# Kernel optimization log

Measured on AMD Instinct MI355X. Metric: run time of the kernel, lower is better.

Reference implementation:

```python
import jax, jax.numpy as jnp
import numpy as np
import math

B, S, D, H = 4, 512, 1024, 16
DH = D // H
DQ = D // 4
MIN_STEPS, MAX_STEPS = 4, 12
THR = 1e-4


def lin(t, w, b):
    # torch Linear convention: w is (out, in)
    return jnp.einsum('...i,oi->...o', t, w) + b


def gelu(t):
    return jax.nn.gelu(t, approximate=False)  # torch nn.GELU() exact


def layernorm(t, g, b):
    m = t.mean(-1, keepdims=True)
    v = jnp.mean(jnp.square(t - m), axis=-1, keepdims=True)
    return (t - m) * jax.lax.rsqrt(v + 1e-5) * g + b


def _forward(h, x, ig_w1, ig_b1, ig_w2, ig_b2, wq, bq, wk, bk, wv, bv, wo, bo,
             g1_w1, g1_b1, g1_w2, g1_b2, gate_logits, ln_g, ln_b,
             sp_w1, sp_b1, sp_w2, sp_b2):
    # adaptive step count: steps = base + floor(sigmoid(MLP(mean_pool(h))).mean() * extra)
    pooled = h.mean(axis=1)  # (B, D)
    extra = jax.nn.sigmoid(lin(gelu(lin(pooled, sp_w1, sp_b1)), sp_w2, sp_b2)).mean()
    num_steps = jnp.minimum(
        MIN_STEPS + jnp.floor(extra * (MAX_STEPS - MIN_STEPS)).astype(jnp.int32), MAX_STEPS)

    gw = jax.nn.softmax(gate_logits)  # gate weights over the 3 gates
    scale = 1.0 / math.sqrt(DH)

    def step(carry, i):
        h, active = carry
        # G1 gate (G2/G3 multiply zero memory/expert outputs -> drop)
        G1 = jax.nn.sigmoid(lin(gelu(lin(h, g1_w1, g1_b1)), g1_w2, g1_b2)) * gw[0]
        # Phi: input-gated blend + raw multi-head self-attention
        gate = jax.nn.sigmoid(
            lin(gelu(lin(jnp.concatenate([h, x], axis=-1), ig_w1, ig_b1)), ig_w2, ig_b2))
        blended = gate * h + (1.0 - gate) * x
        q = lin(blended, wq, bq).reshape(B, S, H, DH)
        k = lin(blended, wk, bk).reshape(B, S, H, DH)
        v = lin(blended, wv, bv).reshape(B, S, H, DH)
        attn = jax.nn.softmax(jnp.einsum('bqhd,bkhd->bhqk', q, k) * scale, axis=-1)
        ctx = jnp.einsum('bhqk,bkhd->bqhd', attn, v).reshape(B, S, D)
        phi = lin(ctx, wo, bo)
        h_new = layernorm(h + G1 * phi, ln_g, ln_b)
        res = jnp.linalg.norm(h_new - h) / (jnp.linalg.norm(h) + 1e-8)
        act_i = active & (i < num_steps)
        h = jnp.where(act_i, h_new, h)
        active = act_i & jnp.logical_not((i >= MIN_STEPS) & (res < THR))
        return (h, active), None

    (h, _), _ = jax.lax.scan(step, (h, jnp.array(True)), jnp.arange(MAX_STEPS))
    return h


def setup_inputs() -> dict:
    key = jax.random.key(0)
    ks = jax.random.split(key, 16)
    f32 = jnp.float32

    def W(k, out_d, in_d):
        return jax.random.normal(k, (out_d, in_d), f32) * (1.0 / np.sqrt(in_d))

    return {
        'h': jax.random.normal(ks[0], (B, S, D), f32),
        'x': jax.random.normal(ks[1], (B, S, D), f32),
        # PhiLayer input_gate: Linear(2D, D/4) -> GELU -> Linear(D/4, D) -> Sigmoid
        'ig_w1': W(ks[2], DQ, 2 * D), 'ig_b1': jnp.zeros((DQ,), f32),
        'ig_w2': W(ks[3], D, DQ), 'ig_b2': jnp.zeros((D,), f32),
        # QKV / out projections (xavier-ish, zero bias)
        'wq': W(ks[4], D, D), 'bq': jnp.zeros((D,), f32),
        'wk': W(ks[5], D, D), 'bk': jnp.zeros((D,), f32),
        'wv': W(ks[6], D, D), 'bv': jnp.zeros((D,), f32),
        'wo': W(ks[7], D, D), 'bo': jnp.zeros((D,), f32),
        # Gating gate #1 MLP (only G1 contributes; memory/experts are zero)
        'g1_w1': W(ks[8], DQ, D), 'g1_b1': jnp.zeros((DQ,), f32),
        'g1_w2': W(ks[9], D, DQ), 'g1_b2': jnp.zeros((D,), f32),
        'gate_logits': jnp.ones((3,), f32),  # nn.Parameter(torch.ones(3))
        # LayerNorm
        'ln_g': jnp.ones((D,), f32), 'ln_b': jnp.zeros((D,), f32),
        # step predictor: Linear(D, D/4) -> GELU -> Linear(D/4, 1)
        'sp_w1': W(ks[10], DQ, D), 'sp_b1': jnp.zeros((DQ,), f32),
        'sp_w2': W(ks[11], 1, DQ), 'sp_b2': jnp.zeros((1,), f32),
    }


def reference(h, x, ig_w1, ig_b1, ig_w2, ig_b2, wq, bq, wk, bk, wv, bv, wo, bo,
              g1_w1, g1_b1, g1_w2, g1_b2, gate_logits, ln_g, ln_b,
              sp_w1, sp_b1, sp_w2, sp_b2):
    return _forward(h, x, ig_w1, ig_b1, ig_w2, ig_b2, wq, bq, wk, bk, wv, bv, wo, bo,
                    g1_w1, g1_b1, g1_w2, g1_b2, gate_logits, ln_g, ln_b,
                    sp_w1, sp_b1, sp_w2, sp_b2)
```

## Files before the change

kernel.cpp:

```cpp
#include <hip/hip_runtime.h>
#include <hip/hip_bf16.h>


#define B_   4
#define S_   512
#define D_   1024
#define H_   16
#define DH_  64
#define MSEQ 2048
#define GRID_ 512

typedef short short8 __attribute__((ext_vector_type(8)));
typedef float floatx4 __attribute__((ext_vector_type(4)));

static constexpr size_t OFF_H    = 0;
static constexpr size_t OFF_X    = 2097152;
static constexpr size_t OFF_HXB  = 4194304;
static constexpr size_t OFF_T2B  = 6291456;
static constexpr size_t OFF_T1B  = 6553600;
static constexpr size_t OFF_G1B  = 6815744;
static constexpr size_t OFF_QKVB = 7864320;
static constexpr size_t OFF_U    = 7864320;
static constexpr size_t OFF_CTXB = 11010048;
static constexpr size_t OFF_WARE = 12058624;
static constexpr size_t OFF_BIAS = 14811136;
static constexpr size_t OFF_POOL = 14817792;
static constexpr size_t OFF_SPT  = 14821888;
static constexpr size_t OFF_PPART= 14822912;
static constexpr size_t OFF_SCAL = 14888448;
static constexpr size_t OFF_XIG  = 14888960;

static constexpr int W_WIG1 = 0;
static constexpr int W_WIG2 = 524288;
static constexpr int W_WG1  = 786432;
static constexpr int W_WG2  = 1048576;
static constexpr int W_QKV  = 1310720;
static constexpr int W_WO   = 4456448;
static constexpr int W_TOT  = 5505024;
static constexpr int B_TOT  = 6656;

__device__ __forceinline__ float bf2f(unsigned int u) {
  return __uint_as_float((u & 0xFFFFu) << 16);
}
__device__ __forceinline__ short f2bs(float f) {
  __hip_bfloat16 b = __float2bfloat16(f);
  return *reinterpret_cast<short*>(&b);
}
__device__ __forceinline__ unsigned int pk2(float lo, float hi) {
  return (unsigned int)(unsigned short)f2bs(lo) | ((unsigned int)(unsigned short)f2bs(hi) << 16);
}
__device__ __forceinline__ float ldf(const void* p, size_t i, int f32m) {
  return f32m ? ((const float*)p)[i] : bf2f(((const unsigned short*)p)[i]);
}
__device__ __forceinline__ int f32mode(const void* lng) {
  return (((const unsigned int*)lng)[0] == 0x3F800000u) ? 1 : 0;
}
__device__ __forceinline__ float gelu_f(float x) {
  return 0.5f * x * (1.0f + erff(x * 0.70710678118654752440f));
}
__device__ __forceinline__ float sig_f(float x) {
  return 1.0f / (1.0f + expf(-x));
}
__device__ __forceinline__ void gl_lds16(const short* gp, short* lp) {
  __builtin_amdgcn_global_load_lds(
      (const __attribute__((address_space(1))) unsigned int*)gp,
      (__attribute__((address_space(3))) unsigned int*)lp, 16, 0, 0);
}
__device__ __forceinline__ float wave_sum(float v) {
  #pragma unroll
  for (int off = 32; off > 0; off >>= 1) v += __shfl_xor(v, off);
  return v;
}

struct RepackPtrs {
  const void* w[8];
  const void* b[8];
};

__global__ __launch_bounds__(256) void repack_all_kernel(
    const void* __restrict__ lng, RepackPtrs ps,
    short* __restrict__ wdst, float* __restrict__ bdst) {
  const int f32m = f32mode(lng);
  int i = blockIdx.x * 256 + threadIdx.x;
  if (i < W_TOT) {
    const int off[9] = {0, 524288, 786432, 1048576, 1310720, 2359296, 3407872, 4456448, W_TOT};
    int seg = 0;
    #pragma unroll
    for (int s = 1; s < 8; s++) seg += (i >= off[s]) ? 1 : 0;
    wdst[i] = f2bs(ldf(ps.w[seg], i - off[seg], f32m));
  } else if (i < W_TOT + B_TOT) {
    int j = i - W_TOT;
    const int off[9] = {0, 256, 1280, 1536, 2560, 3584, 4608, 5632, B_TOT};
    int seg = 0;
    #pragma unroll
    for (int s = 1; s < 8; s++) seg += (j >= off[s]) ? 1 : 0;
    bdst[j] = ldf(ps.b[seg], j - off[seg], f32m);
  }
}

__global__ __launch_bounds__(256) void cvt_in_kernel(
    const void* __restrict__ lng, const void* __restrict__ hb,
    const void* __restrict__ xb, float* __restrict__ h, float* __restrict__ x,
    short* __restrict__ hxb, int n) {
  int f32m = f32mode(lng);
  int i = blockIdx.x * 256 + threadIdx.x;
  if (i < n) {
    float hv = ldf(hb, i, f32m);
    float xv = ldf(xb, i, f32m);
    h[i] = hv;
    x[i] = xv;
    int row = i >> 10, col = i & 1023;
    hxb[(size_t)row * 2048 + col] = f2bs(hv);
    hxb[(size_t)row * 2048 + 1024 + col] = f2bs(xv);
  }
}

__global__ __launch_bounds__(256) void pool_s1_kernel(
    const float* __restrict__ H, float* __restrict__ part) {
  int b = blockIdx.x, c = blockIdx.y, tid = threadIdx.x;
  const float* p = H + ((size_t)b * S_ + c * 32) * D_;
  #pragma unroll
  for (int rep = 0; rep < 4; rep++) {
    int d = rep * 256 + tid;
    float s = 0.f;
    for (int r = 0; r < 32; r++) s += p[(size_t)r * D_ + d];
    part[((size_t)b * 16 + c) * D_ + d] = s;
  }
}
__global__ __launch_bounds__(256) void pool_s2_kernel(
    const float* __restrict__ part, float* __restrict__ pooled) {
  int i = blockIdx.x * 256 + threadIdx.x;
  int b = i >> 10, d = i & 1023;
  float s = 0.f;
  #pragma unroll
  for (int c = 0; c < 16; c++) s += part[((size_t)b * 16 + c) * D_ + d];
  pooled[i] = s * (1.0f / (float)S_);
}

__device__ __forceinline__ float blk_sum256(float v, float* sm, int tid) {
  #pragma unroll
  for (int off = 32; off > 0; off >>= 1) v += __shfl_xor(v, off);
  __syncthreads();
  if ((tid & 63) == 0) sm[tid >> 6] = v;
  __syncthreads();
  return sm[0] + sm[1] + sm[2] + sm[3];
}

__global__ __launch_bounds__(256) void sp1_kernel(
    const void* __restrict__ lng, const float* __restrict__ pooled,
    const void* __restrict__ w1, const void* __restrict__ b1,
    float* __restrict__ spt) {
  __shared__ float sm[4];
  const int f32m = f32mode(lng);
  int j = blockIdx.x, tid = threadIdx.x;
  float s[4] = {0.f, 0.f, 0.f, 0.f};
  #pragma unroll
  for (int r = 0; r < 4; r++) {
    int k = tid * 4 + r;
    float w = ldf(w1, (size_t)j * D_ + k, f32m);
    s[0] += pooled[k] * w;
    s[1] += pooled[1024 + k] * w;
    s[2] += pooled[2048 + k] * w;
    s[3] += pooled[3072 + k] * w;
  }
  #pragma unroll
  for (int b = 0; b < 4; b++) {
    float t = blk_sum256(s[b], sm, tid);
    __syncthreads();
    if (tid == 0) spt[b * 256 + j] = gelu_f(t + ldf(b1, j, f32m));
  }
}

__global__ __launch_bounds__(256) void sp2_kernel(
    const void* __restrict__ lng, const float* __restrict__ spt,
    const void* __restrict__ w2, const void* __restrict__ b2,
    const void* __restrict__ glog,
    int* __restrict__ num_steps, int* __restrict__ active, int* __restrict__ cur,
    float* __restrict__ gw0, float* __restrict__ ssd, float* __restrict__ ssh,
    int* __restrict__ cnt) {
  __shared__ float z[4];
  const int f32m = f32mode(lng);
  int tid = threadIdx.x;
  if (tid < 12) cnt[tid] = 0;
  int wave = tid >> 6, lane = tid & 63;
  {
    int b = wave;
    float s = spt[b * 256 + lane]       * ldf(w2, lane, f32m) +
              spt[b * 256 + lane + 64]  * ldf(w2, lane + 64, f32m) +
              spt[b * 256 + lane + 128] * ldf(w2, lane + 128, f32m) +
              spt[b * 256 + lane + 192] * ldf(w2, lane + 192, f32m);
    #pragma unroll
    for (int off = 32; off > 0; off >>= 1) s += __shfl_xor(s, off);
    if (lane == 0) z[b] = sig_f(s + ldf(b2, 0, f32m));
  }
  __syncthreads();
  if (tid == 0) {
    float extra = 0.25f * (z[0] + z[1] + z[2] + z[3]);
    int ns = 4 + (int)floorf(extra * 8.0f);
    if (ns > 12) ns = 12;
    *num_steps = ns;
    *active = 1;
    *cur = 1;
    *ssd = 0.f; *ssh = 0.f;
    float g0 = ldf(glog, 0, f32m);
    float g1 = ldf(glog, 1, f32m);
    float g2 = ldf(glog, 2, f32m);
    float mx = fmaxf(g0, fmaxf(g1, g2));
    float e0 = expf(g0 - mx), e1 = expf(g1 - mx), e2 = expf(g2 - mx);
    *gw0 = e0 / (e0 + e1 + e2);
  }
}

enum { EPI_NONE = 0, EPI_GELU = 1, EPI_SIGSCALE = 2, EPI_BLEND = 3, EPI_RESADD = 4,
       EPI_GELU_ADD = 5, EPI_F32NB = 6 };

template <int EPI, int BM, int BN>
__device__ __forceinline__ void mgemm_core(
    short* As, short* Bs,
    const short* __restrict__ A, int lda,
    const short* __restrict__ W, int ldw, const float* __restrict__ bias,
    int K, int N,
    float* __restrict__ Cf, short* __restrict__ Cb,
    const float* __restrict__ aux1, const float* __restrict__ aux2f,
    const short* __restrict__ aux2b, const float* __restrict__ scale_ptr,
    int m0, int n0) {
  constexpr int FM = (BM / 2) / 16;
  constexpr int FN = (BN / 2) / 16;
  constexpr int CPA = (BM / 16) / 4;
  constexpr int CPB = (BN / 16) / 4;
  const int tid = threadIdx.x;
  const int lane = tid & 63, wv_ = tid >> 6;
  const int wm = (wv_ >> 1) * (BM / 2), wn = (wv_ & 1) * (BN / 2);
  const int srow = lane >> 2, scol = (lane & 3) * 8;
  const int frow = lane & 15, fk = (lane >> 4) * 8;

  floatx4 acc[FM][FN];
  #pragma unroll
  for (int i = 0; i < FM; i++)
    #pragma unroll
    for (int j = 0; j < FN; j++) acc[i][j] = (floatx4){0.f, 0.f, 0.f, 0.f};

  auto stage = [&](int buf, int k0) {
    short* Ad = As + buf * (BM * 64);
    short* Bd = Bs + buf * (BN * 64);
    #pragma unroll
    for (int c = 0; c < CPA; c++) {
      int q = wv_ * CPA + c;
      const short* gp = A + (size_t)(m0 + q * 16 + srow) * lda + k0 + scol;
      gl_lds16(gp, Ad + q * 512);
      gl_lds16(gp + 32, Ad + BM * 32 + q * 512);
    }
    #pragma unroll
    for (int c = 0; c < CPB; c++) {
      int q = wv_ * CPB + c;
      const short* gp = W + (size_t)(n0 + q * 16 + srow) * ldw + k0 + scol;
      gl_lds16(gp, Bd + q * 512);
      gl_lds16(gp + 32, Bd + BN * 32 + q * 512);
    }
  };

  stage(0, 0);
  __syncthreads();

  int cur = 0;
  for (int k0 = 0; k0 < K; k0 += 64) {
    if (k0 + 64 < K) stage(cur ^ 1, k0 + 64);
    const short* Ab = As + cur * (BM * 64);
    const short* Bb = Bs + cur * (BN * 64);
    #pragma unroll
    for (int hlf = 0; hlf < 2; hlf++) {
      const short* Ah = Ab + hlf * BM * 32;
      const short* Bh = Bb + hlf * BN * 32;
      short8 a[FM], b[FN];
      #pragma unroll
      for (int i = 0; i < FM; i++)
        a[i] = *reinterpret_cast<const short8*>(&Ah[(wm + i * 16 + frow) * 32 + fk]);
      #pragma unroll
      for (int j = 0; j < FN; j++)
        b[j] = *reinterpret_cast<const short8*>(&Bh[(wn + j * 16 + frow) * 32 + fk]);
      #pragma unroll
      for (int i = 0; i < FM; i++)
        #pragma unroll
        for (int j = 0; j < FN; j++)
          acc[i][j] = __builtin_amdgcn_mfma_f32_16x16x32_bf16(a[i], b[j], acc[i][j], 0, 0, 0);
    }
    __syncthreads();
    cur ^= 1;
  }

  float gwv = 0.f;
  if (EPI == EPI_SIGSCALE) gwv = *scale_ptr;
  const int rq = (lane >> 4) * 4;
  #pragma unroll
  for (int i = 0; i < FM; i++) {
    #pragma unroll
    for (int j = 0; j < FN; j++) {
      int n = n0 + wn + j * 16 + (lane & 15);
      float bv = (EPI == EPI_F32NB) ? 0.f : bias[n];
      #pragma unroll
      for (int r = 0; r < 4; r++) {
        int m = m0 + wm + i * 16 + rq + r;
        size_t off = (size_t)m * N + n;
        float v = acc[i][j][r] + bv;
        if (EPI == EPI_GELU) {
          Cb[off] = f2bs(gelu_f(v));
        } else if (EPI == EPI_GELU_ADD) {
          if (aux1) v += aux1[off];
          Cb[off] = f2bs(gelu_f(v));
        } else if (EPI == EPI_SIGSCALE) {
          Cb[off] = f2bs(sig_f(v) * gwv);
        } else if (EPI == EPI_BLEND) {
          float s = sig_f(v);
          Cb[off] = f2bs(s * aux1[off] + (1.f - s) * aux2f[off]);
        } else if (EPI == EPI_RESADD) {
          Cf[off] = aux1[off] + bf2f((unsigned short)aux2b[off]) * v;
        } else if (EPI == EPI_F32NB) {
          Cf[off] = v;
        } else {
          Cb[off] = f2bs(v);
        }
      }
    }
  }
}

template <int EPI, int BM, int BN>
__global__ __launch_bounds__(256) void mgemm(
    const int* __restrict__ flag, const short* __restrict__ A, int lda,
    const short* __restrict__ W, int ldw, const float* __restrict__ bias,
    int K, int N,
    float* __restrict__ Cf, short* __restrict__ Cb,
    const float* __restrict__ aux1, const float* __restrict__ aux2f,
    const short* __restrict__ aux2b, const float* __restrict__ scale_ptr) {
  if (flag && *flag == 0) return;
  __shared__ short As[2 * BM * 64];
  __shared__ short Bs[2 * BN * 64];
  mgemm_core<EPI, BM, BN>(As, Bs, A, lda, W, ldw, bias, K, N, Cf, Cb,
                          aux1, aux2f, aux2b, scale_ptr,
                          blockIdx.y * BM, blockIdx.x * BN);
}

__global__ __launch_bounds__(256) void gate1_kernel(
    const int* __restrict__ flag, const short* __restrict__ hxb,
    const short* __restrict__ warena, const float* __restrict__ biasA,
    short* __restrict__ t2b, short* __restrict__ t1b,
    const float* __restrict__ xig, int kz0) {
  if (*flag == 0) return;
  __shared__ short As[2 * 64 * 64];
  __shared__ short Bs[2 * 64 * 64];
  if (blockIdx.z == 0)
    mgemm_core<EPI_GELU_ADD, 64, 64>(As, Bs, hxb, 2048, warena + W_WIG1, 2048,
                                     biasA + 0, kz0, 256, nullptr, t2b, xig,
                                     nullptr, nullptr, nullptr,
                                     blockIdx.y * 64, blockIdx.x * 64);
  else
    mgemm_core<EPI_GELU, 64, 64>(As, Bs, hxb, 2048, warena + W_WG1, 1024,
                                 biasA + 1280, 1024, 256, nullptr, t1b, nullptr,
                                 nullptr, nullptr, nullptr,
                                 blockIdx.y * 64, blockIdx.x * 64);
}

__global__ __launch_bounds__(256) void gate2_kernel(
    const int* __restrict__ flag, const short* __restrict__ t2b,
    const short* __restrict__ t1b, const short* __restrict__ warena,
    const float* __restrict__ biasA, short* __restrict__ bldb,
    short* __restrict__ g1b, const float* __restrict__ h,
    const float* __restrict__ xf, const float* __restrict__ gw0) {
  if (*flag == 0) return;
  __shared__ short As[2 * 128 * 64];
  __shared__ short Bs[2 * 64 * 64];
  if (blockIdx.z == 0)
    mgemm_core<EPI_BLEND, 128, 64>(As, Bs, t2b, 256, warena + W_WIG2, 256,
                                   biasA + 256, 256, 1024, nullptr, bldb, h, xf,
                                   nullptr, nullptr, blockIdx.y * 128, blockIdx.x * 64);
  else
    mgemm_core<EPI_SIGSCALE, 128, 64>(As, Bs, t1b, 256, warena + W_WG2, 256,
                                      biasA + 1536, 256, 1024, nullptr, g1b,
                                      nullptr, nullptr, nullptr, gw0,
                                      blockIdx.y * 128, blockIdx.x * 64);
}

#define AP_ 72
__global__ __launch_bounds__(256) void attn_kernel(
    const int* __restrict__ flag, const short* __restrict__ qkv,
    short* __restrict__ ctxb) {
  if (*flag == 0) return;
  __shared__ short Ks[64 * AP_];
  __shared__ short Vt[64 * AP_];
  __shared__ short Ps[64 * AP_];
  const int tid = threadIdx.x;
  const int lane = tid & 63, wv = tid >> 6;
  const int ln15 = lane & 15, quad = lane >> 4;
  const int qt = blockIdx.x, hh = blockIdx.y, b = blockIdx.z;
  const int wm = wv * 16;
  const size_t rowbase = (size_t)b * S_;
  const int hcol = hh * DH_;
  const float scale = 0.125f;

  short8 qa[2];
  {
    const short* qp = qkv + (rowbase + qt * 64 + wm + ln15) * 3072 + hcol + quad * 8;
    qa[0] = *reinterpret_cast<const short8*>(qp);
    qa[1] = *reinterpret_cast<const short8*>(qp + 32);
  }
  const int skk = tid >> 2, scg = (tid & 3) * 16;

  float mrow[4] = {-1e30f, -1e30f, -1e30f, -1e30f};
  float lrow[4] = {0.f, 0.f, 0.f, 0.f};
  floatx4 accO[4];
  #pragma unroll
  for (int j = 0; j < 4; j++) accO[j] = (floatx4){0.f, 0.f, 0.f, 0.f};

  for (int kt = 0; kt < 8; kt++) {
    __syncthreads();
    {
      const short* gk = qkv + (rowbase + kt * 64 + skk) * 3072 + 1024 + hcol + scg;
      uint4 k0 = *reinterpret_cast<const uint4*>(gk);
      uint4 k1 = *reinterpret_cast<const uint4*>(gk + 8);
      *reinterpret_cast<uint4*>(&Ks[skk * AP_ + scg]) = k0;
      *reinterpret_cast<uint4*>(&Ks[skk * AP_ + scg + 8]) = k1;
      short8 v0 = *reinterpret_cast<const short8*>(gk + 1024);
      short8 v1 = *reinterpret_cast<const short8*>(gk + 1032);
      #pragma unroll
      for (int j = 0; j < 8; j++) Vt[(scg + j) * AP_ + skk] = v0[j];
      #pragma unroll
      for (int j = 0; j < 8; j++) Vt[(scg + 8 + j) * AP_ + skk] = v1[j];
    }
    __syncthreads();

    floatx4 sc[4];
    #pragma unroll
    for (int nf = 0; nf < 4; nf++) {
      short8 b0 = *reinterpret_cast<const short8*>(&Ks[(nf * 16 + ln15) * AP_ + quad * 8]);
      short8 b1 = *reinterpret_cast<const short8*>(&Ks[(nf * 16 + ln15) * AP_ + 32 + quad * 8]);
      floatx4 s = (floatx4){0.f, 0.f, 0.f, 0.f};
      s = __builtin_amdgcn_mfma_f32_16x16x32_bf16(qa[0], b0, s, 0, 0, 0);
      s = __builtin_amdgcn_mfma_f32_16x16x32_bf16(qa[1], b1, s, 0, 0, 0);
      sc[nf] = s;
    }

    float prob[4][4];
    #pragma unroll
    for (int r = 0; r < 4; r++) {
      float lm = fmaxf(fmaxf(sc[0][r], sc[1][r]), fmaxf(sc[2][r], sc[3][r])) * scale;
      lm = fmaxf(lm, __shfl_xor(lm, 1));
      lm = fmaxf(lm, __shfl_xor(lm, 2));
      lm = fmaxf(lm, __shfl_xor(lm, 4));
      lm = fmaxf(lm, __shfl_xor(lm, 8));
      float mn = fmaxf(mrow[r], lm);
      float alpha = expf(mrow[r] - mn);
      float ls = 0.f;
      #pragma unroll
      for (int nf = 0; nf < 4; nf++) {
        float p = expf(sc[nf][r] * scale - mn);
        prob[nf][r] = p;
        ls += p;
      }
      ls += __shfl_xor(ls, 1);
      ls += __shfl_xor(ls, 2);
      ls += __shfl_xor(ls, 4);
      ls += __shfl_xor(ls, 8);
      lrow[r] = lrow[r] * alpha + ls;
      mrow[r] = mn;
      #pragma unroll
      for (int df = 0; df < 4; df++) accO[df][r] *= alpha;
    }
    #pragma unroll
    for (int nf = 0; nf < 4; nf++)
      #pragma unroll
      for (int r = 0; r < 4; r++)
        Ps[(wm + quad * 4 + r) * AP_ + nf * 16 + ln15] = f2bs(prob[nf][r]);
    __syncthreads();

    short8 pa0 = *reinterpret_cast<const short8*>(&Ps[(wm + ln15) * AP_ + quad * 8]);
    short8 pa1 = *reinterpret_cast<const short8*>(&Ps[(wm + ln15) * AP_ + 32 + quad * 8]);
    #pragma unroll
    for (int df = 0; df < 4; df++) {
      short8 bv0 = *reinterpret_cast<const short8*>(&Vt[(df * 16 + ln15) * AP_ + quad * 8]);
      short8 bv1 = *reinterpret_cast<const short8*>(&Vt[(df * 16 + ln15) * AP_ + 32 + quad * 8]);
      accO[df] = __builtin_amdgcn_mfma_f32_16x16x32_bf16(pa0, bv0, accO[df], 0, 0, 0);
      accO[df] = __builtin_amdgcn_mfma_f32_16x16x32_bf16(pa1, bv1, accO[df], 0, 0, 0);
    }
  }

  float inv[4];
  #pragma unroll
  for (int r = 0; r < 4; r++) inv[r] = 1.0f / lrow[r];
  #pragma unroll
  for (int df = 0; df < 4; df++) {
    #pragma unroll
    for (int r = 0; r < 4; r++) {
      size_t off = (rowbase + qt * 64 + wm + quad * 4 + r) * 1024 + hcol + df * 16 + ln15;
      ctxb[off] = f2bs(accO[df][r] * inv[r]);
    }
  }
}

__global__ __launch_bounds__(256) void ln_kernel(
    int step_i, const int* __restrict__ flagp,
    const float* __restrict__ U, float* __restrict__ H, short* __restrict__ hxb,
    const void* __restrict__ g, const void* __restrict__ be,
    void* __restrict__ Out,
    float* __restrict__ ssd, float* __restrict__ ssh,
    int* __restrict__ active, int* __restrict__ cur,
    const int* __restrict__ num_steps, int* __restrict__ cnt) {
  const int flag = *flagp;
  const int f32m = f32mode(g);
  __shared__ float sdd[4], sdh[4];
  const int tid = threadIdx.x;
  const int wv = tid >> 6, lane = tid & 63;
  if (flag) {
    const int row = blockIdx.x * 4 + wv;
    const float4* u4 = reinterpret_cast<const float4*>(U + (size_t)row * D_);
    float4* h4 = reinterpret_cast<float4*>(H + (size_t)row * D_);
    float4 uv[4], hv[4];
    #pragma unroll
    for (int j = 0; j < 4; j++) uv[j] = u4[lane + 64 * j];
    #pragma unroll
    for (int j = 0; j < 4; j++) hv[j] = h4[lane + 64 * j];
    float s = 0.f;
    #pragma unroll
    for (int j = 0; j < 4; j++) s += (uv[j].x + uv[j].y) + (uv[j].z + uv[j].w);
    s = wave_sum(s);
    float mean = s * (1.0f / (float)D_);
    float4 d[4];
    float vv = 0.f;
    #pragma unroll
    for (int j = 0; j < 4; j++) {
      d[j].x = uv[j].x - mean; d[j].y = uv[j].y - mean;
      d[j].z = uv[j].z - mean; d[j].w = uv[j].w - mean;
      vv += d[j].x * d[j].x + d[j].y * d[j].y + d[j].z * d[j].z + d[j].w * d[j].w;
    }
    vv = wave_sum(vv);
    float rstd = rsqrtf(vv * (1.0f / (float)D_) + 1e-5f);
    float lsd = 0.f, lsh = 0.f;
    #pragma unroll
    for (int j = 0; j < 4; j++) {
      int c = (lane + 64 * j) * 4;
      float hn0 = d[j].x * rstd * ldf(g, c + 0, f32m) + ldf(be, c + 0, f32m);
      float hn1 = d[j].y * rstd * ldf(g, c + 1, f32m) + ldf(be, c + 1, f32m);
      float hn2 = d[j].z * rstd * ldf(g, c + 2, f32m) + ldf(be, c + 2, f32m);
      float hn3 = d[j].w * rstd * ldf(g, c + 3, f32m) + ldf(be, c + 3, f32m);
      float e0 = hn0 - hv[j].x, e1 = hn1 - hv[j].y, e2 = hn2 - hv[j].z, e3 = hn3 - hv[j].w;
      lsd += e0 * e0 + e1 * e1 + e2 * e2 + e3 * e3;
      lsh += hv[j].x * hv[j].x + hv[j].y * hv[j].y + hv[j].z * hv[j].z + hv[j].w * hv[j].w;
      float4 hnv = make_float4(hn0, hn1, hn2, hn3);
      h4[lane + 64 * j] = hnv;
      uint2 pw;
      pw.x = pk2(hn0, hn1);
      pw.y = pk2(hn2, hn3);
      *reinterpret_cast<uint2*>(hxb + (size_t)row * 2048 + c) = pw;
      if (f32m) {
        reinterpret_cast<float4*>(Out)[(size_t)row * 256 + lane + 64 * j] = hnv;
      } else {
        *reinterpret_cast<uint2*>((short*)Out + (size_t)row * 1024 + c) = pw;
      }
    }
    lsd = wave_sum(lsd);
    lsh = wave_sum(lsh);
    if (lane == 0) { sdd[wv] = lsd; sdh[wv] = lsh; }
    __syncthreads();
    if (tid == 0) {
      atomicAdd(ssd, (sdd[0] + sdd[1]) + (sdd[2] + sdd[3]));
      atomicAdd(ssh, (sdh[0] + sdh[1]) + (sdh[2] + sdh[3]));
    }
  }
  if (tid == 0) {
    __threadfence();
    int old = atomicAdd(&cnt[step_i], 1);
    if (old == (int)gridDim.x - 1) {
      if (flag && step_i >= 4) {
        float nd = atomicAdd(ssd, 0.0f);
        float nh = atomicAdd(ssh, 0.0f);
        float res = sqrtf(nd) / (sqrtf(nh) + 1e-8f);
        if (res < 1e-4f) *active = 0;
      }
      *cur = ((*active) && (step_i + 1 < *num_steps)) ? 1 : 0;
      *ssd = 0.f; *ssh = 0.f;
    }
  }
}

extern "C" void kernel_launch(void* const* d_in, const int* in_sizes, int n_in,
                              void* d_out, int out_size, void* d_ws, size_t ws_size,
                              hipStream_t stream) {
  (void)in_sizes; (void)n_in; (void)out_size;
  const void* h_in  = d_in[0];
  const void* x_in  = d_in[1];
  const void* glog  = d_in[18];
  const void* ln_g  = d_in[19];
  const void* ln_b  = d_in[20];
  const void* sp_w1 = d_in[21];
  const void* sp_b1 = d_in[22];
  const void* sp_w2 = d_in[23];
  const void* sp_b2 = d_in[24];

  RepackPtrs rp;
  rp.w[0] = d_in[2];  rp.w[1] = d_in[4];  rp.w[2] = d_in[14]; rp.w[3] = d_in[16];
  rp.w[4] = d_in[6];  rp.w[5] = d_in[8];  rp.w[6] = d_in[10]; rp.w[7] = d_in[12];
  rp.b[0] = d_in[3];  rp.b[1] = d_in[5];  rp.b[2] = d_in[15]; rp.b[3] = d_in[17];
  rp.b[4] = d_in[7];  rp.b[5] = d_in[9];  rp.b[6] = d_in[11]; rp.b[7] = d_in[13];

  float* wsf = (float*)d_ws;
  float* h      = wsf + OFF_H;
  float* xf     = wsf + OFF_X;
  short* hxb    = (short*)(wsf + OFF_HXB);
  short* t2b    = (short*)(wsf + OFF_T2B);
  short* t1b    = (short*)(wsf + OFF_T1B);
  short* g1b    = (short*)(wsf + OFF_G1B);
  short* qkvb   = (short*)(wsf + OFF_QKVB);
  float* u      = wsf + OFF_U;
  short* ctxb   = (short*)(wsf + OFF_CTXB);
  short* bldb   = ctxb;
  short* warena = (short*)(wsf + OFF_WARE);
  float* biasA  = wsf + OFF_BIAS;
  float* pooled = wsf + OFF_POOL;
  float* spt    = wsf + OFF_SPT;
  float* ppart  = wsf + OFF_PPART;
  float* xigf   = wsf + OFF_XIG;
  float* ssd    = wsf + OFF_SCAL + 0;
  float* ssh    = wsf + OFF_SCAL + 1;
  float* gw0    = wsf + OFF_SCAL + 2;
  int* ip        = (int*)(wsf + OFF_SCAL + 8);
  int* num_steps = ip + 0;
  int* active    = ip + 1;
  int* cur       = ip + 2;
  int* cnt       = ip + 4;

  const int NTOT = B_ * S_ * D_;

  const int use_xig = (ws_size >= (OFF_XIG + 524288) * sizeof(float)) ? 1 : 0;
  const int kz0 = use_xig ? 1024 : 2048;

  repack_all_kernel<<<(W_TOT + B_TOT + 255) / 256, 256, 0, stream>>>(ln_g, rp, warena, biasA);
  cvt_in_kernel<<<NTOT / 256, 256, 0, stream>>>(ln_g, h_in, x_in, h, xf, hxb, NTOT);
  if (use_xig) {
    mgemm<EPI_F32NB, 64, 64><<<dim3(4, 32), 256, 0, stream>>>(
        nullptr, hxb + 1024, 2048, warena + W_WIG1 + 1024, 2048, nullptr,
        1024, 256, xigf, nullptr, nullptr, nullptr, nullptr, nullptr);
  }
  pool_s1_kernel<<<dim3(4, 16), 256, 0, stream>>>(h, ppart);
  pool_s2_kernel<<<16, 256, 0, stream>>>(ppart, pooled);
  sp1_kernel<<<256, 256, 0, stream>>>(ln_g, pooled, sp_w1, sp_b1, spt);
  sp2_kernel<<<1, 256, 0, stream>>>(ln_g, spt, sp_w2, sp_b2, glog,
                                    num_steps, active, cur, gw0, ssd, ssh, cnt);

  for (int i = 0; i < 12; i++) {
    gate1_kernel<<<dim3(4, 32, 2), 256, 0, stream>>>(
        cur, hxb, warena, biasA, t2b, t1b, use_xig ? xigf : nullptr, kz0);
    gate2_kernel<<<dim3(16, 16, 2), 256, 0, stream>>>(cur, t2b, t1b, warena, biasA,
                                                      bldb, g1b, h, xf, gw0);
    mgemm<EPI_NONE, 128, 64><<<dim3(48, 16), 256, 0, stream>>>(
        cur, bldb, 1024, warena + W_QKV, 1024, biasA + 2560, 1024, 3072,
        nullptr, qkvb, nullptr, nullptr, nullptr, nullptr);
    attn_kernel<<<dim3(8, 16, 4), 256, 0, stream>>>(cur, qkvb, ctxb);
    mgemm<EPI_RESADD, 64, 64><<<dim3(16, 32), 256, 0, stream>>>(
        cur, ctxb, 1024, warena + W_WO, 1024, biasA + 5632, 1024, 1024,
        u, nullptr, h, nullptr, g1b, nullptr);
    ln_kernel<<<512, 256, 0, stream>>>(i, cur, u, h, hxb, ln_g, ln_b, d_out,
                                       ssd, ssh, active, cur, num_steps, cnt);
  }
}
```

Measured before the change: 1.153 ms.

## Double-buffer K/V tiles in attention with register prefetch and fewer barriers

Result: no change. 1.150 ms, median of 2 (-0.2%).

```diff
diff --git a/kernel.cpp b/kernel.cpp
--- a/kernel.cpp
+++ b/kernel.cpp
@@ -385,8 +385,8 @@
     const int* __restrict__ flag, const short* __restrict__ qkv,
     short* __restrict__ ctxb) {
   if (*flag == 0) return;
-  __shared__ short Ks[64 * AP_];
-  __shared__ short Vt[64 * AP_];
+  __shared__ short Ks[2][64 * AP_];
+  __shared__ short Vt[2][64 * AP_];
   __shared__ short Ps[64 * AP_];
   const int tid = threadIdx.x;
   const int lane = tid & 63, wv = tid >> 6;
@@ -411,28 +411,37 @@
   #pragma unroll
   for (int j = 0; j < 4; j++) accO[j] = (floatx4){0.f, 0.f, 0.f, 0.f};
 
+  uint4 rk0, rk1;
+  short8 rv0, rv1;
+  auto load_regs = [&](int kt) {
+    const short* gk = qkv + (rowbase + kt * 64 + skk) * 3072 + 1024 + hcol + scg;
+    rk0 = *reinterpret_cast<const uint4*>(gk);
+    rk1 = *reinterpret_cast<const uint4*>(gk + 8);
+    rv0 = *reinterpret_cast<const short8*>(gk + 1024);
+    rv1 = *reinterpret_cast<const short8*>(gk + 1032);
+  };
+  auto write_lds = [&](int buf) {
+    *reinterpret_cast<uint4*>(&Ks[buf][skk * AP_ + scg]) = rk0;
+    *reinterpret_cast<uint4*>(&Ks[buf][skk * AP_ + scg + 8]) = rk1;
+    #pragma unroll
+    for (int j = 0; j < 8; j++) Vt[buf][(scg + j) * AP_ + skk] = rv0[j];
+    #pragma unroll
+    for (int j = 0; j < 8; j++) Vt[buf][(scg + 8 + j) * AP_ + skk] = rv1[j];
+  };
+
+  load_regs(0);
+  write_lds(0);
+  __syncthreads();
+
+  int cur = 0;
   for (int kt = 0; kt < 8; kt++) {
-    __syncthreads();
-    {
-      const short* gk = qkv + (rowbase + kt * 64 + skk) * 3072 + 1024 + hcol + scg;
-      uint4 k0 = *reinterpret_cast<const uint4*>(gk);
-      uint4 k1 = *reinterpret_cast<const uint4*>(gk + 8);
-      *reinterpret_cast<uint4*>(&Ks[skk * AP_ + scg]) = k0;
-      *reinterpret_cast<uint4*>(&Ks[skk * AP_ + scg + 8]) = k1;
-      short8 v0 = *reinterpret_cast<const short8*>(gk + 1024);
-      short8 v1 = *reinterpret_cast<const short8*>(gk + 1032);
-      #pragma unroll
-      for (int j = 0; j < 8; j++) Vt[(scg + j) * AP_ + skk] = v0[j];
-      #pragma unroll
-      for (int j = 0; j < 8; j++) Vt[(scg + 8 + j) * AP_ + skk] = v1[j];
-    }
-    __syncthreads();
+    if (kt < 7) load_regs(kt + 1);
 
     floatx4 sc[4];
     #pragma unroll
     for (int nf = 0; nf < 4; nf++) {
-      short8 b0 = *reinterpret_cast<const short8*>(&Ks[(nf * 16 + ln15) * AP_ + quad * 8]);
-      short8 b1 = *reinterpret_cast<const short8*>(&Ks[(nf * 16 + ln15) * AP_ + 32 + quad * 8]);
+      short8 b0 = *reinterpret_cast<const short8*>(&Ks[cur][(nf * 16 + ln15) * AP_ + quad * 8]);
+      short8 b1 = *reinterpret_cast<const short8*>(&Ks[cur][(nf * 16 + ln15) * AP_ + 32 + quad * 8]);
       floatx4 s = (floatx4){0.f, 0.f, 0.f, 0.f};
       s = __builtin_amdgcn_mfma_f32_16x16x32_bf16(qa[0], b0, s, 0, 0, 0);
       s = __builtin_amdgcn_mfma_f32_16x16x32_bf16(qa[1], b1, s, 0, 0, 0);
@@ -470,17 +479,20 @@
       #pragma unroll
       for (int r = 0; r < 4; r++)
         Ps[(wm + quad * 4 + r) * AP_ + nf * 16 + ln15] = f2bs(prob[nf][r]);
-    __syncthreads();
 
     short8 pa0 = *reinterpret_cast<const short8*>(&Ps[(wm + ln15) * AP_ + quad * 8]);
     short8 pa1 = *reinterpret_cast<const short8*>(&Ps[(wm + ln15) * AP_ + 32 + quad * 8]);
     #pragma unroll
     for (int df = 0; df < 4; df++) {
-      short8 bv0 = *reinterpret_cast<const short8*>(&Vt[(df * 16 + ln15) * AP_ + quad * 8]);
-      short8 bv1 = *reinterpret_cast<const short8*>(&Vt[(df * 16 + ln15) * AP_ + 32 + quad * 8]);
+      short8 bv0 = *reinterpret_cast<const short8*>(&Vt[cur][(df * 16 + ln15) * AP_ + quad * 8]);
+      short8 bv1 = *reinterpret_cast<const short8*>(&Vt[cur][(df * 16 + ln15) * AP_ + 32 + quad * 8]);
       accO[df] = __builtin_amdgcn_mfma_f32_16x16x32_bf16(pa0, bv0, accO[df], 0, 0, 0);
       accO[df] = __builtin_amdgcn_mfma_f32_16x16x32_bf16(pa1, bv1, accO[df], 0, 0, 0);
     }
+
+    if (kt < 7) write_lds(cur ^ 1);
+    __syncthreads();
+    cur ^= 1;
   }
 
   float inv[4];
```
